# Optimization experiments

Measured on AMD Instinct MI355X. Metric: run time of the kernel, lower is better.

Reference implementation:

```python
import jax, jax.numpy as jnp
import numpy as np

NUM_GROUPS = 32
EPS = 1e-6


def group_norm(x, weight, bias):
    # x: [b, c, h, w]
    b, c, h, w = x.shape
    xg = x.reshape(b, NUM_GROUPS, c // NUM_GROUPS, h, w)
    mean = jnp.mean(xg, axis=(2, 3, 4), keepdims=True)
    var = jnp.var(xg, axis=(2, 3, 4), keepdims=True)
    xn = ((xg - mean) * jax.lax.rsqrt(var + EPS)).reshape(b, c, h, w)
    return xn * weight[None, :, None, None] + bias[None, :, None, None]


def conv1x1(x, w, b):
    # 1x1 conv == per-pixel matmul. x: [b, c_in, h, w], w: [c_out, c_in]
    return jnp.einsum('oi,bihw->bohw', w, x) + b[None, :, None, None]


def setup_inputs() -> dict:
    key = jax.random.key(0)
    ks = jax.random.split(key, 9)
    b, c, h, w = 8, 512, 64, 64
    scale = 1.0 / np.sqrt(c)
    return {
        'x': jax.random.normal(ks[0], (b, c, h, w), jnp.float32),
        'gn_weight': jnp.ones((c,), jnp.float32),
        'gn_bias': jnp.zeros((c,), jnp.float32),
        'wq': jax.random.normal(ks[1], (c, c), jnp.float32) * scale,
        'bq': jnp.zeros((c,), jnp.float32),
        'wk': jax.random.normal(ks[2], (c, c), jnp.float32) * scale,
        'bk': jnp.zeros((c,), jnp.float32),
        'wv': jax.random.normal(ks[3], (c, c), jnp.float32) * scale,
        'bv': jnp.zeros((c,), jnp.float32),
        'wp': jax.random.normal(ks[4], (c, c), jnp.float32) * scale,
        'bp': jnp.zeros((c,), jnp.float32),
    }


def reference(x, gn_weight, gn_bias, wq, bq, wk, bk, wv, bv, wp, bp):
    h_ = group_norm(x, gn_weight, gn_bias)
    q = conv1x1(h_, wq, bq)
    k = conv1x1(h_, wk, bk)
    v = conv1x1(h_, wv, bv)
    b, c, h, w = q.shape
    n = h * w
    qf = q.reshape(b, c, n)
    kf = k.reshape(b, c, n)
    vf = v.reshape(b, c, n)
    # scores: [b, q, k]
    scores = jnp.einsum('bcq,bck->bqk', qf, kf) * (c ** -0.5)
    attn = jax.nn.softmax(scores, axis=-1)
    out = jnp.einsum('bqk,bck->bcq', attn, vf).reshape(b, c, h, w)
    out = conv1x1(out, wp, bp)
    return x + out
```

## Files before the change

### kernel.cpp

```cpp
#include <hip/hip_runtime.h>
#include <cstdint>

typedef unsigned short u16;
typedef __bf16 bf16x8 __attribute__((ext_vector_type(8)));
typedef float f32x4 __attribute__((ext_vector_type(4)));

__device__ __forceinline__ u16 f2bf(float f) {
    uint32_t u = __float_as_uint(f);
    u += 0x7FFFu + ((u >> 16) & 1u);
    return (u16)(u >> 16);
}
__device__ __forceinline__ float bf2f(u16 v) {
    return __uint_as_float((uint32_t)v << 16);
}

__device__ __forceinline__ void gload16(const u16* g, u16* l) {
    __builtin_amdgcn_global_load_lds(
        (const __attribute__((address_space(1))) uint32_t*)g,
        (__attribute__((address_space(3))) uint32_t*)l, 16, 0, 0);
}

__device__ __forceinline__ void swz(int& n_idx, int& m_idx, int& z_idx) {
    const int nx = gridDim.x, ny = gridDim.y;
    int lid = blockIdx.x + nx * (blockIdx.y + ny * blockIdx.z);
    int g = lid & 7, h = lid >> 3;
    n_idx = h % nx;
    int pair = (h / nx) * 8 + g;
    m_idx = pair % ny;
    z_idx = pair / ny;
}

__global__ __launch_bounds__(256) void k_detect(const u16* __restrict__ x,
                                                int* __restrict__ flag) {
    const int t = threadIdx.x;
    uint32_t mx = 0;
    for (int i = 0; i < 256; i++) {
        uint32_t v = (uint32_t)x[i * 256 + t] & 0x7FFFu;
        mx = mx > v ? mx : v;
    }
    for (int off = 32; off > 0; off >>= 1) {
        uint32_t o = (uint32_t)__shfl_xor((int)mx, off);
        mx = mx > o ? mx : o;
    }
    __shared__ uint32_t r[4];
    if ((t & 63) == 0) r[t >> 6] = mx;
    __syncthreads();
    if (t == 0) {
        uint32_t a = r[0] > r[1] ? r[0] : r[1];
        uint32_t b = r[2] > r[3] ? r[2] : r[3];
        mx = a > b ? a : b;
        *flag = (mx > 0x5000u) ? 1 : 0;
    }
}

__global__ __launch_bounds__(256) void k_cvt_wb(const void* wq, const void* wk,
                                                const void* wv, const void* wp,
                                                const void* gw, const void* gb,
                                                const void* bq, const void* bk,
                                                const void* bv, const void* bp,
                                                const int* __restrict__ flag,
                                                u16* __restrict__ Wc,
                                                u16* __restrict__ Bc) {
    const int mode = *flag;
    int i = blockIdx.x * 256 + threadIdx.x;
    if (i >= 1048576 + 3072) return;
    const void* src;
    u16* dst;
    int off;
    if (i < 1048576) {
        int which = i >> 18;
        off = i & 262143;
        src = which == 0 ? wq : which == 1 ? wk : which == 2 ? wv : wp;
        dst = Wc + i;
    } else {
        int j = i - 1048576;
        int which = j >> 9;
        off = j & 511;
        src = which == 0 ? gw : which == 1 ? gb : which == 2 ? bq
            : which == 3 ? bk : which == 4 ? bv : bp;
        dst = Bc + j;
    }
    *dst = mode ? f2bf(((const float*)src)[off]) : ((const u16*)src)[off];
}

__global__ __launch_bounds__(256) void k_gn_stats(const void* __restrict__ x_raw,
                                                  const u16* __restrict__ Bc,
                                                  const int* __restrict__ flag,
                                                  float* __restrict__ Sc,
                                                  float* __restrict__ Sh) {
    const int b = blockIdx.x >> 5, g = blockIdx.x & 31;
    const int mode = *flag;
    const int t = threadIdx.x;
    const int wave = t >> 6, lane = t & 63;
    float s = 0.f, ss = 0.f;
    if (mode) {
        const float4* xb = (const float4*)((const float*)x_raw +
                                           ((size_t)b * 512 + g * 16) * 4096);
        for (int it = 0; it < 64; it++) {
            float4 v = xb[it * 256 + t];
            s += v.x + v.y + v.z + v.w;
            ss += v.x * v.x + v.y * v.y + v.z * v.z + v.w * v.w;
        }
    } else {
        const uint4* xb = (const uint4*)((const u16*)x_raw +
                                         ((size_t)b * 512 + g * 16) * 4096);
        for (int it = 0; it < 32; it++) {
            uint4 v = xb[it * 256 + t];
            uint32_t w[4] = {v.x, v.y, v.z, v.w};
            for (int j = 0; j < 4; j++) {
                float a = __uint_as_float(w[j] << 16);
                float c = __uint_as_float(w[j] & 0xFFFF0000u);
                s += a + c;
                ss += a * a + c * c;
            }
        }
    }
    for (int off = 32; off > 0; off >>= 1) {
        s += __shfl_xor(s, off);
        ss += __shfl_xor(ss, off);
    }
    __shared__ float rs[4], rss[4];
    if (lane == 0) { rs[wave] = s; rss[wave] = ss; }
    __syncthreads();
    s = rs[0] + rs[1] + rs[2] + rs[3];
    ss = rss[0] + rss[1] + rss[2] + rss[3];
    const float mean = s * (1.f / 65536.f);
    const float var = ss * (1.f / 65536.f) - mean * mean;
    const float rstd = rsqrtf(var + 1e-6f);
    if (t < 16) {
        int c = g * 16 + t;
        float w = bf2f(Bc[c]);
        Sc[b * 512 + c] = rstd * w;
        Sh[b * 512 + c] = bf2f(Bc[512 + c]) - mean * rstd * w;
    }
}

#define TPAD 520
__global__ __launch_bounds__(256) void k_gn_apply(const void* __restrict__ x_raw,
                                                  const int* __restrict__ flag,
                                                  const float* __restrict__ Sc,
                                                  const float* __restrict__ Sh,
                                                  u16* __restrict__ HT) {
    __shared__ u16 tile[64 * TPAD];
    __shared__ float sSc[512], sSh[512];
    const int b = blockIdx.y;
    const int p0 = blockIdx.x * 64;
    const int mode = *flag;
    const int t = threadIdx.x;
    sSc[t] = Sc[b * 512 + t]; sSc[t + 256] = Sc[b * 512 + t + 256];
    sSh[t] = Sh[b * 512 + t]; sSh[t + 256] = Sh[b * 512 + t + 256];
    __syncthreads();
    for (int it = 0; it < 16; it++) {
        int li = it * 256 + t;
        int c = li >> 3;
        int pj = (li & 7) * 8;
        float v[8];
        if (mode) {
            const float* xr = (const float*)x_raw + ((size_t)b * 512 + c) * 4096 + p0 + pj;
            float4 a = *(const float4*)xr;
            float4 d = *(const float4*)(xr + 4);
            v[0] = a.x; v[1] = a.y; v[2] = a.z; v[3] = a.w;
            v[4] = d.x; v[5] = d.y; v[6] = d.z; v[7] = d.w;
        } else {
            const u16* xr = (const u16*)x_raw + ((size_t)b * 512 + c) * 4096 + p0 + pj;
            uint4 a = *(const uint4*)xr;
            uint32_t w[4] = {a.x, a.y, a.z, a.w};
            for (int j = 0; j < 4; j++) {
                v[2 * j] = __uint_as_float(w[j] << 16);
                v[2 * j + 1] = __uint_as_float(w[j] & 0xFFFF0000u);
            }
        }
        float sc = sSc[c], sh = sSh[c];
        for (int k = 0; k < 8; k++)
            tile[(pj + k) * TPAD + c] = f2bf(v[k] * sc + sh);
    }
    __syncthreads();
    u16* H = HT + (size_t)b * 2097152 + (size_t)p0 * 512;
    for (int it = 0; it < 16; it++) {
        int ch = it * 256 + t;
        int pp = ch >> 6;
        int cc = (ch & 63) * 8;
        *(uint4*)&H[(size_t)pp * 512 + cc] = *(const uint4*)&tile[pp * TPAD + cc];
    }
}

__device__ __forceinline__ void gemm_core(const u16* __restrict__ A,
                                          const u16* __restrict__ BT,
                                          int lda, int ldb, int K,
                                          int m0, int n0,
                                          u16* lA, u16* lB,
                                          f32x4 (&acc)[4][4]) {
    const int t = threadIdx.x;
    const int wave = t >> 6, lane = t & 63;
    const int wm = (wave >> 1) * 64, wn = (wave & 1) * 64;
    const int mf = lane & 15, quad = lane >> 4;
    const int srow = t >> 3;
    const int scol = (((t & 7) ^ (srow & 7)) * 8);
    const u16* Ap = A + (size_t)(m0 + srow) * lda + scol;
    const u16* Bp = BT + (size_t)(n0 + srow) * ldb + scol;
    u16* lAd = &lA[t * 8];
    u16* lBd = &lB[t * 8];
    const int fx = mf & 7;

    for (int i = 0; i < 4; i++)
        for (int j = 0; j < 4; j++)
            acc[i][j] = (f32x4){0.f, 0.f, 0.f, 0.f};

    for (int k0 = 0; k0 < K; k0 += 64) {
        __syncthreads();
        gload16(Ap + k0, lAd);
        gload16(Ap + k0 + (size_t)32 * lda, lAd + 2048);
        gload16(Ap + k0 + (size_t)64 * lda, lAd + 4096);
        gload16(Ap + k0 + (size_t)96 * lda, lAd + 6144);
        gload16(Bp + k0, lBd);
        gload16(Bp + k0 + (size_t)32 * ldb, lBd + 2048);
        gload16(Bp + k0 + (size_t)64 * ldb, lBd + 4096);
        gload16(Bp + k0 + (size_t)96 * ldb, lBd + 6144);
        __syncthreads();
        for (int ks = 0; ks < 2; ks++) {
            bf16x8 af[4], bfr[4];
            const int sl = ((ks * 4 + quad) ^ fx) * 8;
            for (int i = 0; i < 4; i++)
                af[i] = *(const bf16x8*)&lA[(wm + i * 16 + mf) * 64 + sl];
            for (int j = 0; j < 4; j++)
                bfr[j] = *(const bf16x8*)&lB[(wn + j * 16 + mf) * 64 + sl];
            for (int i = 0; i < 4; i++)
                for (int j = 0; j < 4; j++)
                    acc[i][j] = __builtin_amdgcn_mfma_f32_16x16x32_bf16(af[i], bfr[j], acc[i][j], 0, 0, 0);
        }
    }
}

__global__ __launch_bounds__(256) void k_qk(const u16* __restrict__ HT,
                                            const u16* __restrict__ Wc,
                                            const u16* __restrict__ Bc,
                                            u16* __restrict__ QT,
                                            u16* __restrict__ KT) {
    __shared__ __align__(16) u16 lds[24576];
    int nI, mI, b;
    swz(nI, mI, b);
    const int n0 = nI * 128;
    const int m0 = mI * 128;
    const u16* A = HT + (size_t)b * 2097152;
    const u16* biasq = Bc + 1024;
    const u16* biask = Bc + 1024 + 512;
    u16* lA = lds;
    u16* lBq = lds + 8192;
    u16* lBk = lds + 16384;

    const int t = threadIdx.x;
    const int wave = t >> 6, lane = t & 63;
    const int wm = (wave >> 1) * 64, wn = (wave & 1) * 64;
    const int mf = lane & 15, quad = lane >> 4;
    const int srow = t >> 3;
    const int scol = (((t & 7) ^ (srow & 7)) * 8);
    const u16* Ap = A + (size_t)(m0 + srow) * 512 + scol;
    const u16* Bqp = Wc + (size_t)(n0 + srow) * 512 + scol;
    const u16* Bkp = Wc + 262144 + (size_t)(n0 + srow) * 512 + scol;
    u16* lAd = lA + t * 8;
    u16* lBqd = lBq + t * 8;
    u16* lBkd = lBk + t * 8;
    const int fx = mf & 7;

    f32x4 aq[4][4], ak[4][4];
    for (int i = 0; i < 4; i++)
        for (int j = 0; j < 4; j++) {
            aq[i][j] = (f32x4){0.f, 0.f, 0.f, 0.f};
            ak[i][j] = (f32x4){0.f, 0.f, 0.f, 0.f};
        }

    for (int k0 = 0; k0 < 512; k0 += 64) {
        __syncthreads();
        gload16(Ap + k0, lAd);
        gload16(Ap + k0 + (size_t)32 * 512, lAd + 2048);
        gload16(Ap + k0 + (size_t)64 * 512, lAd + 4096);
        gload16(Ap + k0 + (size_t)96 * 512, lAd + 6144);
        gload16(Bqp + k0, lBqd);
        gload16(Bqp + k0 + (size_t)32 * 512, lBqd + 2048);
        gload16(Bqp + k0 + (size_t)64 * 512, lBqd + 4096);
        gload16(Bqp + k0 + (size_t)96 * 512, lBqd + 6144);
        gload16(Bkp + k0, lBkd);
        gload16(Bkp + k0 + (size_t)32 * 512, lBkd + 2048);
        gload16(Bkp + k0 + (size_t)64 * 512, lBkd + 4096);
        gload16(Bkp + k0 + (size_t)96 * 512, lBkd + 6144);
        __syncthreads();
#pragma unroll
        for (int ks = 0; ks < 2; ks++) {
            bf16x8 af[4], bq4[4], bk4[4];
            const int sl = ((ks * 4 + quad) ^ fx) * 8;
#pragma unroll
            for (int i = 0; i < 4; i++)
                af[i] = *(const bf16x8*)&lA[(wm + i * 16 + mf) * 64 + sl];
#pragma unroll
            for (int j = 0; j < 4; j++) {
                bq4[j] = *(const bf16x8*)&lBq[(wn + j * 16 + mf) * 64 + sl];
                bk4[j] = *(const bf16x8*)&lBk[(wn + j * 16 + mf) * 64 + sl];
            }
#pragma unroll
            for (int i = 0; i < 4; i++)
#pragma unroll
                for (int j = 0; j < 4; j++) {
                    aq[i][j] = __builtin_amdgcn_mfma_f32_16x16x32_bf16(af[i], bq4[j], aq[i][j], 0, 0, 0);
                    ak[i][j] = __builtin_amdgcn_mfma_f32_16x16x32_bf16(af[i], bk4[j], ak[i][j], 0, 0, 0);
                }
        }
    }

    for (int which = 0; which < 2; which++) {
        const u16* Bb = which == 0 ? biasq : biask;
        u16* O = (which == 0 ? QT : KT) + (size_t)b * 2097152;
        __syncthreads();
        for (int i = 0; i < 4; i++)
            for (int r = 0; r < 4; r++) {
                int row = wm + i * 16 + quad * 4 + r;
                int kk = ((row >> 2) & 3) << 4;
                for (int j = 0; j < 4; j++) {
                    int col = wn + j * 16 + mf;
                    float v = (which == 0 ? aq[i][j][r] : ak[i][j][r]) + bf2f(Bb[n0 + col]);
                    lds[row * 128 + (col ^ kk)] = f2bf(v);
                }
            }
        __syncthreads();
        for (int p = 0; p < 8; p++) {
            int idx = p * 256 + t;
            int rowt = idx >> 4, c8 = (idx & 15) * 8;
            int kk = ((rowt >> 2) & 3) << 4;
            uint4 v = *(const uint4*)&lds[rowt * 128 + (c8 ^ kk)];
            *(uint4*)&O[(size_t)(m0 + rowt) * 512 + n0 + c8] = v;
        }
    }
}

__global__ __launch_bounds__(256) void k_v(const u16* __restrict__ HT,
                                           const u16* __restrict__ Wc,
                                           const u16* __restrict__ Bc,
                                           u16* __restrict__ V) {
    __shared__ __align__(16) u16 sm[16384];
    int nI, mI, b;
    swz(nI, mI, b);
    const int m0 = nI * 128;
    const int n0 = mI * 128;
    const u16* A = Wc + (size_t)2 * 262144;
    const u16* BT = HT + (size_t)b * 2097152;
    const u16* Bb = Bc + 1024 + 2 * 512;
    u16* O = V + (size_t)b * 2097152;
    f32x4 acc[4][4];
    gemm_core(A, BT, 512, 512, 512, m0, n0, sm, sm + 8192, acc);

    const int t = threadIdx.x;
    const int wave = t >> 6, lane = t & 63;
    const int wm = (wave >> 1) * 64, wn = (wave & 1) * 64;
    const int mf = lane & 15, quad = lane >> 4;
    __syncthreads();
    for (int i = 0; i < 4; i++)
        for (int r = 0; r < 4; r++) {
            int row = wm + i * 16 + quad * 4 + r;
            int kk = ((row >> 2) & 3) << 4;
            float bias = bf2f(Bb[m0 + row]);
            for (int j = 0; j < 4; j++) {
                int col = wn + j * 16 + mf;
                sm[row * 128 + (col ^ kk)] = f2bf(acc[i][j][r] + bias);
            }
        }
    __syncthreads();
    for (int p = 0; p < 8; p++) {
        int idx = p * 256 + t;
        int rowt = idx >> 4, c8 = (idx & 15) * 8;
        int kk = ((rowt >> 2) & 3) << 4;
        uint4 v = *(const uint4*)&sm[rowt * 128 + (c8 ^ kk)];
        *(uint4*)&O[(size_t)(m0 + rowt) * 4096 + n0 + c8] = v;
    }
}

__device__ __forceinline__ u16* s_ptr(u16* S_ht, u16* S_tail, int l) {
    return l == 0 ? S_ht : S_tail + (size_t)(l - 1) * 16777216;
}

__global__ __launch_bounds__(256) void k_scores(const u16* __restrict__ QT,
                                                const u16* __restrict__ KT,
                                                u16* __restrict__ S_ht,
                                                u16* __restrict__ S_tail,
                                                float* __restrict__ Part,
                                                int b0) {
    __shared__ __align__(16) u16 sm[16384];
    int nI, mI, l;
    swz(nI, mI, l);
    const int n0 = nI * 128;
    const int m0 = mI * 128;
    const int b = b0 + l;
    f32x4 acc[4][4];
    gemm_core(QT + (size_t)b * 2097152, KT + (size_t)b * 2097152, 512, 512, 512,
              m0, n0, sm, sm + 8192, acc);

    const float scale = 0.04419417382415922f;
    const int t = threadIdx.x;
    const int wave = t >> 6, lane = t & 63;
    const int wm = (wave >> 1) * 64, wn = (wave & 1) * 64;
    const int mf = lane & 15, quad = lane >> 4;
    __syncthreads();
    for (int i = 0; i < 4; i++)
        for (int r = 0; r < 4; r++) {
            int row = wm + i * 16 + quad * 4 + r;
            int kk = ((row >> 2) & 3) << 4;
            for (int j = 0; j < 4; j++) {
                int col = wn + j * 16 + mf;
                sm[row * 128 + (col ^ kk)] = f2bf(__expf(acc[i][j][r] * scale));
            }
        }
    __syncthreads();
    u16* Sb = s_ptr(S_ht, S_tail, l);
    float* pr = Part + ((size_t)b * 32 + nI) * 4096 + m0;
    for (int p = 0; p < 8; p++) {
        int idx = p * 256 + t;
        int rowt = idx >> 4, c8 = (idx & 15) * 8;
        int kk = ((rowt >> 2) & 3) << 4;
        uint4 v = *(const uint4*)&sm[rowt * 128 + (c8 ^ kk)];
        uint32_t w[4] = {v.x, v.y, v.z, v.w};
        float s = 0.f;
        for (int q2 = 0; q2 < 4; q2++)
            s += __uint_as_float(w[q2] << 16) + __uint_as_float(w[q2] & 0xFFFF0000u);
        for (int off = 8; off > 0; off >>= 1) s += __shfl_xor(s, off);
        if ((lane & 15) == 0) pr[rowt] = s;
        *(uint4*)&Sb[(size_t)(m0 + rowt) * 4096 + n0 + c8] = v;
    }
}

__global__ __launch_bounds__(256) void k_pv_split(u16* __restrict__ S_ht,
                                                  u16* __restrict__ S_tail,
                                                  const u16* __restrict__ V,
                                                  u16* __restrict__ QT,
                                                  u16* __restrict__ KT,
                                                  int b0) {
    __shared__ __align__(16) u16 sm[16384];
    int nI, mI, zI;
    swz(nI, mI, zI);
    const int n0 = nI * 128;
    const int m0 = mI * 128;
    const int l = zI >> 1, split = zI & 1, b = b0 + l;
    const u16* A = s_ptr(S_ht, S_tail, l) + split * 2048;
    const u16* BT = V + (size_t)b * 2097152 + split * 2048;
    f32x4 acc[4][4];
    gemm_core(A, BT, 4096, 4096, 2048, m0, n0, sm, sm + 8192, acc);

    const int t = threadIdx.x;
    const int wave = t >> 6, lane = t & 63;
    const int wm = (wave >> 1) * 64, wn = (wave & 1) * 64;
    const int mf = lane & 15, quad = lane >> 4;
    u16* P = (split == 0 ? QT : KT) + (size_t)b * 2097152;
    __syncthreads();
    for (int i = 0; i < 4; i++)
        for (int r = 0; r < 4; r++) {
            int row = wm + i * 16 + quad * 4 + r;
            int kk = ((row >> 2) & 3) << 4;
            for (int j = 0; j < 4; j++) {
                int col = wn + j * 16 + mf;
                sm[row * 128 + (col ^ kk)] = f2bf(acc[i][j][r]);
            }
        }
    __syncthreads();
    for (int p = 0; p < 8; p++) {
        int idx = p * 256 + t;
        int rowt = idx >> 4, c8 = (idx & 15) * 8;
        int kk = ((rowt >> 2) & 3) << 4;
        uint4 v = *(const uint4*)&sm[rowt * 128 + (c8 ^ kk)];
        *(uint4*)&P[(size_t)(m0 + rowt) * 512 + n0 + c8] = v;
    }
}

__global__ __launch_bounds__(256) void k_pv_reduce(const u16* __restrict__ QT,
                                                   const u16* __restrict__ KT,
                                                   const float* __restrict__ Part,
                                                   u16* __restrict__ OT,
                                                   int b0) {
    const int b = b0 + blockIdx.y;
    const int t = threadIdx.x;
    __shared__ float sInv[4];
    if (t < 128) {
        int r = t >> 5, which = t & 31;
        int p = blockIdx.x * 4 + r;
        float v = Part[((size_t)b * 32 + which) * 4096 + p];
        for (int off = 16; off > 0; off >>= 1) v += __shfl_xor(v, off);
        if (which == 0) sInv[r] = 1.f / v;
    }
    __syncthreads();
    const float inv = sInv[t >> 6];
    size_t base = (size_t)b * 2097152;
    size_t i0 = base + ((size_t)blockIdx.x * 256 + t) * 8;
    uint4 a = *(const uint4*)(QT + i0);
    uint4 c = *(const uint4*)(KT + i0);
    uint32_t wa[4] = {a.x, a.y, a.z, a.w};
    uint32_t wc[4] = {c.x, c.y, c.z, c.w};
    uint32_t o[4];
    for (int j = 0; j < 4; j++) {
        float lo = (__uint_as_float(wa[j] << 16) + __uint_as_float(wc[j] << 16)) * inv;
        float hi = (__uint_as_float(wa[j] & 0xFFFF0000u) + __uint_as_float(wc[j] & 0xFFFF0000u)) * inv;
        o[j] = (uint32_t)f2bf(lo) | ((uint32_t)f2bf(hi) << 16);
    }
    *(uint4*)(OT + i0) = make_uint4(o[0], o[1], o[2], o[3]);
}

__global__ __launch_bounds__(256) void k_proj(const u16* __restrict__ Wc,
                                              const u16* __restrict__ OT,
                                              const u16* __restrict__ Bc,
                                              const void* __restrict__ x_raw,
                                              const int* __restrict__ flag,
                                              void* __restrict__ y_raw) {
    __shared__ __align__(16) u16 smu[16384];
    float* smf = (float*)smu;
    int nI, mI, b;
    swz(nI, mI, b);
    const int n0 = nI * 128;
    const int m0 = mI * 128;
    f32x4 acc[4][4];
    gemm_core(Wc + (size_t)3 * 262144, OT + (size_t)b * 2097152, 512, 512, 512,
              m0, n0, smu, smu + 8192, acc);

    const int mode = *flag;
    const u16* bp = Bc + 5 * 512;
    const int t = threadIdx.x;
    const int wave = t >> 6, lane = t & 63;
    const int wn = (wave & 1) * 64;
    const int mf = lane & 15, quad = lane >> 4;
    const int whalf = wave >> 1;
    size_t bb = (size_t)b * 2097152;
    for (int h = 0; h < 2; h++) {
        __syncthreads();
        if (whalf == h) {
            for (int i = 0; i < 4; i++)
                for (int r = 0; r < 4; r++) {
                    int rowl = i * 16 + quad * 4 + r;
                    int kf = ((rowl >> 2) & 1) << 4;
                    for (int j = 0; j < 4; j++) {
                        int col = wn + j * 16 + mf;
                        smf[rowl * 128 + (col ^ kf)] = acc[i][j][r];
                    }
                }
        }
        __syncthreads();
        const int rowbase = m0 + h * 64;
        if (mode) {
            for (int p = 0; p < 8; p++) {
                int idx = p * 256 + t;
                int rowl = idx >> 5, c4 = (idx & 31) * 4;
                int kf = ((rowl >> 2) & 1) << 4;
                f32x4 v = *(const f32x4*)&smf[rowl * 128 + (c4 ^ kf)];
                int rowg = rowbase + rowl;
                float bias = bf2f(bp[rowg]);
                size_t o = bb + (size_t)rowg * 4096 + n0 + c4;
                float4 xv = *(const float4*)((const float*)x_raw + o);
                float4 out = make_float4(v[0] + bias + xv.x, v[1] + bias + xv.y,
                                         v[2] + bias + xv.z, v[3] + bias + xv.w);
                *(float4*)((float*)y_raw + o) = out;
            }
        } else {
            for (int p = 0; p < 4; p++) {
                int idx = p * 256 + t;
                int rowl = idx >> 4, c8 = (idx & 15) * 8;
                int kf = ((rowl >> 2) & 1) << 4;
                const float* sp = &smf[rowl * 128 + (c8 ^ kf)];
                f32x4 v0 = *(const f32x4*)sp;
                f32x4 v1 = *(const f32x4*)(sp + 4);
                int rowg = rowbase + rowl;
                float bias = bf2f(bp[rowg]);
                size_t o = bb + (size_t)rowg * 4096 + n0 + c8;
                uint4 xv = *(const uint4*)((const u16*)x_raw + o);
                uint32_t xw[4] = {xv.x, xv.y, xv.z, xv.w};
                float vals[8] = {v0[0], v0[1], v0[2], v0[3],
                                 v1[0], v1[1], v1[2], v1[3]};
                uint32_t ow[4];
                for (int q2 = 0; q2 < 4; q2++) {
                    float lo = __uint_as_float(xw[q2] << 16) + vals[2 * q2] + bias;
                    float hi = __uint_as_float(xw[q2] & 0xFFFF0000u) + vals[2 * q2 + 1] + bias;
                    ow[q2] = (uint32_t)f2bf(lo) | ((uint32_t)f2bf(hi) << 16);
                }
                *(uint4*)((u16*)y_raw + o) = make_uint4(ow[0], ow[1], ow[2], ow[3]);
            }
        }
    }
}

extern "C" void kernel_launch(void* const* d_in, const int* in_sizes, int n_in,
                              void* d_out, int out_size, void* d_ws, size_t ws_size,
                              hipStream_t stream) {
    (void)in_sizes; (void)n_in; (void)out_size;
    const void* x  = d_in[0];
    const void* gw = d_in[1];
    const void* gb = d_in[2];
    const void* wq = d_in[3];
    const void* bq = d_in[4];
    const void* wk = d_in[5];
    const void* bk = d_in[6];
    const void* wv = d_in[7];
    const void* bv = d_in[8];
    const void* wp = d_in[9];
    const void* bp = d_in[10];

    u16* ws16 = (u16*)d_ws;
    int* flag = (int*)d_ws;
    float* Sc = (float*)(ws16 + 16);
    float* Sh = Sc + 4096;
    u16* Wc = ws16 + 16 + 16384;
    u16* Bc = Wc + 1048576;
    u16* HT = Bc + 4096;
    u16* QT = HT + 16777216;
    u16* KT = QT + 16777216;
    u16* V  = KT + 16777216;
    u16* OT = V  + 16777216;
    float* Part = (float*)(OT + 16777216);
    u16* Tail = (u16*)(Part + 1048576);
    const size_t base_elems = (size_t)(Tail - ws16);

    int nb = 1;
    for (int cand = 8; cand >= 2; cand >>= 1) {
        size_t need = 2ull * (base_elems + (size_t)(cand - 1) * 16777216ull);
        if (ws_size >= need) { nb = cand; break; }
    }

    k_detect<<<1, 256, 0, stream>>>((const u16*)x, flag);
    k_cvt_wb<<<4108, 256, 0, stream>>>(wq, wk, wv, wp, gw, gb, bq, bk, bv, bp,
                                       flag, Wc, Bc);
    k_gn_stats<<<256, 256, 0, stream>>>(x, Bc, flag, Sc, Sh);
    k_gn_apply<<<dim3(64, 8), 256, 0, stream>>>(x, flag, Sc, Sh, HT);
    k_qk<<<dim3(4, 32, 8), 256, 0, stream>>>(HT, Wc, Bc, QT, KT);
    k_v<<<dim3(4, 32, 8), 256, 0, stream>>>(HT, Wc, Bc, V);
    for (int b0 = 0; b0 < 8; b0 += nb) {
        k_scores<<<dim3(32, 32, nb), 256, 0, stream>>>(QT, KT, HT, Tail, Part, b0);
        k_pv_split<<<dim3(4, 32, 2 * nb), 256, 0, stream>>>(HT, Tail, V, QT, KT, b0);
        k_pv_reduce<<<dim3(1024, nb), 256, 0, stream>>>(QT, KT, Part, OT, b0);
    }
    k_proj<<<dim3(32, 4, 8), 256, 0, stream>>>(Wc, OT, Bc, x, flag, d_out);
}
```

Measured before the change: 799.3 us.

## Use 512-thread blocks computing 128x256 tiles sharing A tile across two B halves

Introduces a gemm_dual helper where 8 waves share one LDS-staged A tile and each half of the block multiplies it against a different 128-column B tile. k_qk, k_scores, k_pv_split and k_proj switch to 512-thread blocks with 128x256 output tiles, halving grid sizes and cutting A-tile reloads from global memory. The aim is more data reuse per LDS load and fewer per-block accumulator registers in k_qk. The trade-offs are fewer blocks, which can leave CUs idle on small grids, and serialized epilogues that need extra barriers.

```diff
diff --git a/kernel.cpp b/kernel.cpp
--- a/kernel.cpp
+++ b/kernel.cpp
@@ -231,98 +231,102 @@
     }
 }
 
-__global__ __launch_bounds__(256) void k_qk(const u16* __restrict__ HT,
-                                            const u16* __restrict__ Wc,
-                                            const u16* __restrict__ Bc,
-                                            u16* __restrict__ QT,
-                                            u16* __restrict__ KT) {
+__device__ __forceinline__ void gemm_dual(const u16* __restrict__ A,
+                                          const u16* __restrict__ B0,
+                                          const u16* __restrict__ B1,
+                                          int lda, int ldb, int K,
+                                          int m0, int n0,
+                                          u16* lds,
+                                          f32x4 (&acc)[4][4]) {
+    const int t = threadIdx.x;
+    const int wave = t >> 6, lane = t & 63;
+    const int half = wave >> 2, wIn = wave & 3;
+    const int wm = (wIn >> 1) * 64, wn = (wIn & 1) * 64;
+    const int mf = lane & 15, quad = lane >> 4;
+    const int srow = t >> 3;
+    const int scol = (((t & 7) ^ (srow & 7)) * 8);
+    const u16* Ap = A + (size_t)(m0 + srow) * lda + scol;
+    const u16* B0p = B0 + (size_t)(n0 + srow) * ldb + scol;
+    const u16* B1p = B1 + (size_t)(n0 + srow) * ldb + scol;
+    u16* lA = lds;
+    u16* lB0 = lds + 8192;
+    u16* lB1 = lds + 16384;
+    u16* lAd = lA + t * 8;
+    u16* lB0d = lB0 + t * 8;
+    u16* lB1d = lB1 + t * 8;
+    const int fx = mf & 7;
+    const u16* lBh = half ? lB1 : lB0;
+
+    for (int i = 0; i < 4; i++)
+        for (int j = 0; j < 4; j++)
+            acc[i][j] = (f32x4){0.f, 0.f, 0.f, 0.f};
+
+    for (int k0 = 0; k0 < K; k0 += 64) {
+        __syncthreads();
+        gload16(Ap + k0, lAd);
+        gload16(Ap + k0 + (size_t)64 * lda, lAd + 4096);
+        gload16(B0p + k0, lB0d);
+        gload16(B0p + k0 + (size_t)64 * ldb, lB0d + 4096);
+        gload16(B1p + k0, lB1d);
+        gload16(B1p + k0 + (size_t)64 * ldb, lB1d + 4096);
+        __syncthreads();
+#pragma unroll
+        for (int ks = 0; ks < 2; ks++) {
+            bf16x8 af[4], bfr[4];
+            const int sl = ((ks * 4 + quad) ^ fx) * 8;
+#pragma unroll
+            for (int i = 0; i < 4; i++)
+                af[i] = *(const bf16x8*)&lA[(wm + i * 16 + mf) * 64 + sl];
+#pragma unroll
+            for (int j = 0; j < 4; j++)
+                bfr[j] = *(const bf16x8*)&lBh[(wn + j * 16 + mf) * 64 + sl];
+#pragma unroll
+            for (int i = 0; i < 4; i++)
+#pragma unroll
+                for (int j = 0; j < 4; j++)
+                    acc[i][j] = __builtin_amdgcn_mfma_f32_16x16x32_bf16(af[i], bfr[j], acc[i][j], 0, 0, 0);
+        }
+    }
+}
+
+__global__ __launch_bounds__(512, 4) void k_qk(const u16* __restrict__ HT,
+                                               const u16* __restrict__ Wc,
+                                               const u16* __restrict__ Bc,
+                                               u16* __restrict__ QT,
+                                               u16* __restrict__ KT) {
     __shared__ __align__(16) u16 lds[24576];
     int nI, mI, b;
     swz(nI, mI, b);
     const int n0 = nI * 128;
     const int m0 = mI * 128;
-    const u16* A = HT + (size_t)b * 2097152;
-    const u16* biasq = Bc + 1024;
-    const u16* biask = Bc + 1024 + 512;
-    u16* lA = lds;
-    u16* lBq = lds + 8192;
-    u16* lBk = lds + 16384;
-
-    const int t = threadIdx.x;
-    const int wave = t >> 6, lane = t & 63;
-    const int wm = (wave >> 1) * 64, wn = (wave & 1) * 64;
+    f32x4 acc[4][4];
+    gemm_dual(HT + (size_t)b * 2097152, Wc, Wc + 262144,
+              512, 512, 512, m0, n0, lds, acc);
+
+    const int t = threadIdx.x;
+    const int wave = t >> 6, lane = t & 63;
+    const int half = wave >> 2, wIn = wave & 3;
+    const int wm = (wIn >> 1) * 64, wn = (wIn & 1) * 64;
     const int mf = lane & 15, quad = lane >> 4;
-    const int srow = t >> 3;
-    const int scol = (((t & 7) ^ (srow & 7)) * 8);
-    const u16* Ap = A + (size_t)(m0 + srow) * 512 + scol;
-    const u16* Bqp = Wc + (size_t)(n0 + srow) * 512 + scol;
-    const u16* Bkp = Wc + 262144 + (size_t)(n0 + srow) * 512 + scol;
-    u16* lAd = lA + t * 8;
-    u16* lBqd = lBq + t * 8;
-    u16* lBkd = lBk + t * 8;
-    const int fx = mf & 7;
-
-    f32x4 aq[4][4], ak[4][4];
-    for (int i = 0; i < 4; i++)
-        for (int j = 0; j < 4; j++) {
-            aq[i][j] = (f32x4){0.f, 0.f, 0.f, 0.f};
-            ak[i][j] = (f32x4){0.f, 0.f, 0.f, 0.f};
-        }
-
-    for (int k0 = 0; k0 < 512; k0 += 64) {
-        __syncthreads();
-        gload16(Ap + k0, lAd);
-        gload16(Ap + k0 + (size_t)32 * 512, lAd + 2048);
-        gload16(Ap + k0 + (size_t)64 * 512, lAd + 4096);
-        gload16(Ap + k0 + (size_t)96 * 512, lAd + 6144);
-        gload16(Bqp + k0, lBqd);
-        gload16(Bqp + k0 + (size_t)32 * 512, lBqd + 2048);
-        gload16(Bqp + k0 + (size_t)64 * 512, lBqd + 4096);
-        gload16(Bqp + k0 + (size_t)96 * 512, lBqd + 6144);
-        gload16(Bkp + k0, lBkd);
-        gload16(Bkp + k0 + (size_t)32 * 512, lBkd + 2048);
-        gload16(Bkp + k0 + (size_t)64 * 512, lBkd + 4096);
-        gload16(Bkp + k0 + (size_t)96 * 512, lBkd + 6144);
-        __syncthreads();
-#pragma unroll
-        for (int ks = 0; ks < 2; ks++) {
-            bf16x8 af[4], bq4[4], bk4[4];
-            const int sl = ((ks * 4 + quad) ^ fx) * 8;
-#pragma unroll
+    for (int which = 0; which < 2; which++) {
+        const u16* Bb = Bc + 1024 + which * 512;
+        u16* O = (which == 0 ? QT : KT) + (size_t)b * 2097152;
+        __syncthreads();
+        if (half == which) {
             for (int i = 0; i < 4; i++)
-                af[i] = *(const bf16x8*)&lA[(wm + i * 16 + mf) * 64 + sl];
-#pragma unroll
-            for (int j = 0; j < 4; j++) {
-                bq4[j] = *(const bf16x8*)&lBq[(wn + j * 16 + mf) * 64 + sl];
-                bk4[j] = *(const bf16x8*)&lBk[(wn + j * 16 + mf) * 64 + sl];
-            }
-#pragma unroll
-            for (int i = 0; i < 4; i++)
-#pragma unroll
-                for (int j = 0; j < 4; j++) {
-                    aq[i][j] = __builtin_amdgcn_mfma_f32_16x16x32_bf16(af[i], bq4[j], aq[i][j], 0, 0, 0);
-                    ak[i][j] = __builtin_amdgcn_mfma_f32_16x16x32_bf16(af[i], bk4[j], ak[i][j], 0, 0, 0);
+                for (int r = 0; r < 4; r++) {
+                    int row = wm + i * 16 + quad * 4 + r;
+                    int kk = ((row >> 2) & 3) << 4;
+                    for (int j = 0; j < 4; j++) {
+                        int col = wn + j * 16 + mf;
+                        lds[row * 128 + (col ^ kk)] =
+                            f2bf(acc[i][j][r] + bf2f(Bb[n0 + col]));
+                    }
                 }
         }
-    }
-
-    for (int which = 0; which < 2; which++) {
-        const u16* Bb = which == 0 ? biasq : biask;
-        u16* O = (which == 0 ? QT : KT) + (size_t)b * 2097152;
-        __syncthreads();
-        for (int i = 0; i < 4; i++)
-            for (int r = 0; r < 4; r++) {
-                int row = wm + i * 16 + quad * 4 + r;
-                int kk = ((row >> 2) & 3) << 4;
-                for (int j = 0; j < 4; j++) {
-                    int col = wn + j * 16 + mf;
-                    float v = (which == 0 ? aq[i][j][r] : ak[i][j][r]) + bf2f(Bb[n0 + col]);
-                    lds[row * 128 + (col ^ kk)] = f2bf(v);
-                }
-            }
-        __syncthreads();
-        for (int p = 0; p < 8; p++) {
-            int idx = p * 256 + t;
+        __syncthreads();
+        for (int p = 0; p < 4; p++) {
+            int idx = p * 512 + t;
             int rowt = idx >> 4, c8 = (idx & 15) * 8;
             int kk = ((rowt >> 2) & 3) << 4;
             uint4 v = *(const uint4*)&lds[rowt * 128 + (c8 ^ kk)];
@@ -376,94 +380,107 @@
     return l == 0 ? S_ht : S_tail + (size_t)(l - 1) * 16777216;
 }
 
-__global__ __launch_bounds__(256) void k_scores(const u16* __restrict__ QT,
-                                                const u16* __restrict__ KT,
-                                                u16* __restrict__ S_ht,
-                                                u16* __restrict__ S_tail,
-                                                float* __restrict__ Part,
-                                                int b0) {
-    __shared__ __align__(16) u16 sm[16384];
+__global__ __launch_bounds__(512, 4) void k_scores(const u16* __restrict__ QT,
+                                                   const u16* __restrict__ KT,
+                                                   u16* __restrict__ S_ht,
+                                                   u16* __restrict__ S_tail,
+                                                   float* __restrict__ Part,
+                                                   int b0) {
+    __shared__ __align__(16) u16 lds[24576];
     int nI, mI, l;
     swz(nI, mI, l);
-    const int n0 = nI * 128;
+    const int n0 = nI * 256;
     const int m0 = mI * 128;
     const int b = b0 + l;
+    const u16* Kb = KT + (size_t)b * 2097152;
     f32x4 acc[4][4];
-    gemm_core(QT + (size_t)b * 2097152, KT + (size_t)b * 2097152, 512, 512, 512,
-              m0, n0, sm, sm + 8192, acc);
+    gemm_dual(QT + (size_t)b * 2097152, Kb + (size_t)n0 * 512,
+              Kb + (size_t)(n0 + 128) * 512, 512, 512, 512, m0, 0, lds, acc);
 
     const float scale = 0.04419417382415922f;
     const int t = threadIdx.x;
     const int wave = t >> 6, lane = t & 63;
-    const int wm = (wave >> 1) * 64, wn = (wave & 1) * 64;
+    const int half = wave >> 2, wIn = wave & 3;
+    const int wm = (wIn >> 1) * 64, wn = (wIn & 1) * 64;
     const int mf = lane & 15, quad = lane >> 4;
-    __syncthreads();
-    for (int i = 0; i < 4; i++)
-        for (int r = 0; r < 4; r++) {
-            int row = wm + i * 16 + quad * 4 + r;
-            int kk = ((row >> 2) & 3) << 4;
-            for (int j = 0; j < 4; j++) {
-                int col = wn + j * 16 + mf;
-                sm[row * 128 + (col ^ kk)] = f2bf(__expf(acc[i][j][r] * scale));
-            }
-        }
-    __syncthreads();
     u16* Sb = s_ptr(S_ht, S_tail, l);
-    float* pr = Part + ((size_t)b * 32 + nI) * 4096 + m0;
-    for (int p = 0; p < 8; p++) {
-        int idx = p * 256 + t;
-        int rowt = idx >> 4, c8 = (idx & 15) * 8;
-        int kk = ((rowt >> 2) & 3) << 4;
-        uint4 v = *(const uint4*)&sm[rowt * 128 + (c8 ^ kk)];
-        uint32_t w[4] = {v.x, v.y, v.z, v.w};
-        float s = 0.f;
-        for (int q2 = 0; q2 < 4; q2++)
-            s += __uint_as_float(w[q2] << 16) + __uint_as_float(w[q2] & 0xFFFF0000u);
-        for (int off = 8; off > 0; off >>= 1) s += __shfl_xor(s, off);
-        if ((lane & 15) == 0) pr[rowt] = s;
-        *(uint4*)&Sb[(size_t)(m0 + rowt) * 4096 + n0 + c8] = v;
-    }
-}
-
-__global__ __launch_bounds__(256) void k_pv_split(u16* __restrict__ S_ht,
-                                                  u16* __restrict__ S_tail,
-                                                  const u16* __restrict__ V,
-                                                  u16* __restrict__ QT,
-                                                  u16* __restrict__ KT,
-                                                  int b0) {
-    __shared__ __align__(16) u16 sm[16384];
+    for (int which = 0; which < 2; which++) {
+        __syncthreads();
+        if (half == which) {
+            for (int i = 0; i < 4; i++)
+                for (int r = 0; r < 4; r++) {
+                    int row = wm + i * 16 + quad * 4 + r;
+                    int kk = ((row >> 2) & 3) << 4;
+                    for (int j = 0; j < 4; j++) {
+                        int col = wn + j * 16 + mf;
+                        lds[row * 128 + (col ^ kk)] =
+                            f2bf(__expf(acc[i][j][r] * scale));
+                    }
+                }
+        }
+        __syncthreads();
+        float* pr = Part + ((size_t)b * 32 + nI * 2 + which) * 4096 + m0;
+        for (int p = 0; p < 4; p++) {
+            int idx = p * 512 + t;
+            int rowt = idx >> 4, c8 = (idx & 15) * 8;
+            int kk = ((rowt >> 2) & 3) << 4;
+            uint4 v = *(const uint4*)&lds[rowt * 128 + (c8 ^ kk)];
+            uint32_t w[4] = {v.x, v.y, v.z, v.w};
+            float s = 0.f;
+            for (int q2 = 0; q2 < 4; q2++)
+                s += __uint_as_float(w[q2] << 16) + __uint_as_float(w[q2] & 0xFFFF0000u);
+            for (int off = 8; off > 0; off >>= 1) s += __shfl_xor(s, off);
+            if ((lane & 15) == 0) pr[rowt] = s;
+            *(uint4*)&Sb[(size_t)(m0 + rowt) * 4096 + n0 + which * 128 + c8] = v;
+        }
+    }
+}
+
+__global__ __launch_bounds__(512, 4) void k_pv_split(u16* __restrict__ S_ht,
+                                                     u16* __restrict__ S_tail,
+                                                     const u16* __restrict__ V,
+                                                     u16* __restrict__ QT,
+                                                     u16* __restrict__ KT,
+                                                     int b0) {
+    __shared__ __align__(16) u16 lds[24576];
     int nI, mI, zI;
     swz(nI, mI, zI);
-    const int n0 = nI * 128;
+    const int n0 = nI * 256;
     const int m0 = mI * 128;
     const int l = zI >> 1, split = zI & 1, b = b0 + l;
     const u16* A = s_ptr(S_ht, S_tail, l) + split * 2048;
-    const u16* BT = V + (size_t)b * 2097152 + split * 2048;
+    const u16* Vb = V + (size_t)b * 2097152 + split * 2048;
     f32x4 acc[4][4];
-    gemm_core(A, BT, 4096, 4096, 2048, m0, n0, sm, sm + 8192, acc);
-
-    const int t = threadIdx.x;
-    const int wave = t >> 6, lane = t & 63;
-    const int wm = (wave >> 1) * 64, wn = (wave & 1) * 64;
+    gemm_dual(A, Vb + (size_t)n0 * 4096, Vb + (size_t)(n0 + 128) * 4096,
+              4096, 4096, 2048, m0, 0, lds, acc);
+
+    const int t = threadIdx.x;
+    const int wave = t >> 6, lane = t & 63;
+    const int half = wave >> 2, wIn = wave & 3;
+    const int wm = (wIn >> 1) * 64, wn = (wIn & 1) * 64;
     const int mf = lane & 15, quad = lane >> 4;
     u16* P = (split == 0 ? QT : KT) + (size_t)b * 2097152;
-    __syncthreads();
-    for (int i = 0; i < 4; i++)
-        for (int r = 0; r < 4; r++) {
-            int row = wm + i * 16 + quad * 4 + r;
-            int kk = ((row >> 2) & 3) << 4;
-            for (int j = 0; j < 4; j++) {
-                int col = wn + j * 16 + mf;
-                sm[row * 128 + (col ^ kk)] = f2bf(acc[i][j][r]);
-            }
-        }
-    __syncthreads();
-    for (int p = 0; p < 8; p++) {
-        int idx = p * 256 + t;
-        int rowt = idx >> 4, c8 = (idx & 15) * 8;
-        int kk = ((rowt >> 2) & 3) << 4;
-        uint4 v = *(const uint4*)&sm[rowt * 128 + (c8 ^ kk)];
-        *(uint4*)&P[(size_t)(m0 + rowt) * 512 + n0 + c8] = v;
+    for (int which = 0; which < 2; which++) {
+        __syncthreads();
+        if (half == which) {
+            for (int i = 0; i < 4; i++)
+                for (int r = 0; r < 4; r++) {
+                    int row = wm + i * 16 + quad * 4 + r;
+                    int kk = ((row >> 2) & 3) << 4;
+                    for (int j = 0; j < 4; j++) {
+                        int col = wn + j * 16 + mf;
+                        lds[row * 128 + (col ^ kk)] = f2bf(acc[i][j][r]);
+                    }
+                }
+        }
+        __syncthreads();
+        for (int p = 0; p < 4; p++) {
+            int idx = p * 512 + t;
+            int rowt = idx >> 4, c8 = (idx & 15) * 8;
+            int kk = ((rowt >> 2) & 3) << 4;
+            uint4 v = *(const uint4*)&lds[rowt * 128 + (c8 ^ kk)];
+            *(uint4*)&P[(size_t)(m0 + rowt) * 512 + n0 + which * 128 + c8] = v;
+        }
     }
 }
 
@@ -499,81 +516,86 @@
     *(uint4*)(OT + i0) = make_uint4(o[0], o[1], o[2], o[3]);
 }
 
-__global__ __launch_bounds__(256) void k_proj(const u16* __restrict__ Wc,
-                                              const u16* __restrict__ OT,
-                                              const u16* __restrict__ Bc,
-                                              const void* __restrict__ x_raw,
-                                              const int* __restrict__ flag,
-                                              void* __restrict__ y_raw) {
-    __shared__ __align__(16) u16 smu[16384];
-    float* smf = (float*)smu;
+__global__ __launch_bounds__(512, 4) void k_proj(const u16* __restrict__ Wc,
+                                                 const u16* __restrict__ OT,
+                                                 const u16* __restrict__ Bc,
+                                                 const void* __restrict__ x_raw,
+                                                 const int* __restrict__ flag,
+                                                 void* __restrict__ y_raw) {
+    __shared__ __align__(16) u16 lds[24576];
+    float* smf = (float*)lds;
     int nI, mI, b;
     swz(nI, mI, b);
-    const int n0 = nI * 128;
+    const int n0 = nI * 256;
     const int m0 = mI * 128;
+    const u16* Ob = OT + (size_t)b * 2097152;
     f32x4 acc[4][4];
-    gemm_core(Wc + (size_t)3 * 262144, OT + (size_t)b * 2097152, 512, 512, 512,
-              m0, n0, smu, smu + 8192, acc);
+    gemm_dual(Wc + (size_t)3 * 262144, Ob + (size_t)n0 * 512,
+              Ob + (size_t)(n0 + 128) * 512, 512, 512, 512, m0, 0, lds, acc);
 
     const int mode = *flag;
     const u16* bp = Bc + 5 * 512;
     const int t = threadIdx.x;
     const int wave = t >> 6, lane = t & 63;
-    const int wn = (wave & 1) * 64;
+    const int half = wave >> 2, wIn = wave & 3;
+    const int wn = (wIn & 1) * 64;
     const int mf = lane & 15, quad = lane >> 4;
-    const int whalf = wave >> 1;
+    const int whalfIn = wIn >> 1;
     size_t bb = (size_t)b * 2097152;
-    for (int h = 0; h < 2; h++) {
-        __syncthreads();
-        if (whalf == h) {
-            for (int i = 0; i < 4; i++)
-                for (int r = 0; r < 4; r++) {
-                    int rowl = i * 16 + quad * 4 + r;
+    for (int which = 0; which < 2; which++) {
+        const int colbase = n0 + which * 128;
+        for (int h = 0; h < 2; h++) {
+            __syncthreads();
+            if (half == which && whalfIn == h) {
+                for (int i = 0; i < 4; i++)
+                    for (int r = 0; r < 4; r++) {
+                        int rowl = i * 16 + quad * 4 + r;
+                        int kf = ((rowl >> 2) & 1) << 4;
+                        for (int j = 0; j < 4; j++) {
+                            int col = wn + j * 16 + mf;
+                            smf[rowl * 128 + (col ^ kf)] = acc[i][j][r];
+                        }
+                    }
+            }
+            __syncthreads();
+            const int rowbase = m0 + h * 64;
+            if (mode) {
+                for (int p = 0; p < 4; p++) {
+                    int idx = p * 512 + t;
+                    int rowl = idx >> 5, c4 = (idx & 31) * 4;
                     int kf = ((rowl >> 2) & 1) << 4;
-                    for (int j = 0; j < 4; j++) {
-                        int col = wn + j * 16 + mf;
-                        smf[rowl * 128 + (col ^ kf)] = acc[i][j][r];
+                    f32x4 v = *(const f32x4*)&smf[rowl * 128 + (c4 ^ kf)];
+                    int rowg = rowbase + rowl;
+                    float bias = bf2f(bp[rowg]);
+                    size_t o = bb + (size_t)rowg * 4096 + colbase + c4;
+                    float4 xv = *(const float4*)((const float*)x_raw + o);
+                    float4 out = make_float4(v[0] + bias + xv.x, v[1] + bias + xv.y,
+                                             v[2] + bias + xv.z, v[3] + bias + xv.w);
+                    *(float4*)((float*)y_raw + o) = out;
+                }
+            } else {
+                for (int p = 0; p < 2; p++) {
+                    int idx = p * 512 + t;
+                    int rowl = idx >> 4, c8 = (idx & 15) * 8;
+                    int kf = ((rowl >> 2) & 1) << 4;
+                    const float* sp = &smf[rowl * 128 + (c8 ^ kf)];
+                    f32x4 v0 = *(const f32x4*)sp;
+                    f32x4 v1 = *(const f32x4*)(sp + 4);
+                    int rowg = rowbase + rowl;
+                    float bias = bf2f(bp[rowg]);
+                    size_t o = bb + (size_t)rowg * 4096 + colbase + c8;
+                    uint4 xv = *(const uint4*)((const u16*)x_raw + o);
+                    uint32_t xw[4] = {xv.x, xv.y, xv.z, xv.w};
+                    float vals[8] = {v0[0], v0[1], v0[2], v0[3],
+                                     v1[0], v1[1], v1[2], v1[3]};
+                    uint32_t ow[4];
+                    for (int q2 = 0; q2 < 4; q2++) {
+                        float lo = __uint_as_float(xw[q2] << 16) + vals[2 * q2] + bias;
+                        float hi = __uint_as_float(xw[q2] & 0xFFFF0000u) + vals[2 * q2 + 1] + bias;
+                        ow[q2] = (uint32_t)f2bf(lo) | ((uint32_t)f2bf(hi) << 16);
                     }
+                    *(uint4*)((u16*)y_raw + o) = make_uint4(ow[0], ow[1], ow[2], ow[3]);
                 }
-        }
-        __syncthreads();
-        const int rowbase = m0 + h * 64;
-        if (mode) {
-            for (int p = 0; p < 8; p++) {
-                int idx = p * 256 + t;
-                int rowl = idx >> 5, c4 = (idx & 31) * 4;
-                int kf = ((rowl >> 2) & 1) << 4;
-                f32x4 v = *(const f32x4*)&smf[rowl * 128 + (c4 ^ kf)];
-                int rowg = rowbase + rowl;
-                float bias = bf2f(bp[rowg]);
-                size_t o = bb + (size_t)rowg * 4096 + n0 + c4;
-                float4 xv = *(const float4*)((const float*)x_raw + o);
-                float4 out = make_float4(v[0] + bias + xv.x, v[1] + bias + xv.y,
-                                         v[2] + bias + xv.z, v[3] + bias + xv.w);
-                *(float4*)((float*)y_raw + o) = out;
-            }
-        } else {
-            for (int p = 0; p < 4; p++) {
-                int idx = p * 256 + t;
-                int rowl = idx >> 4, c8 = (idx & 15) * 8;
-                int kf = ((rowl >> 2) & 1) << 4;
-                const float* sp = &smf[rowl * 128 + (c8 ^ kf)];
-                f32x4 v0 = *(const f32x4*)sp;
-                f32x4 v1 = *(const f32x4*)(sp + 4);
-                int rowg = rowbase + rowl;
-                float bias = bf2f(bp[rowg]);
-                size_t o = bb + (size_t)rowg * 4096 + n0 + c8;
-                uint4 xv = *(const uint4*)((const u16*)x_raw + o);
-                uint32_t xw[4] = {xv.x, xv.y, xv.z, xv.w};
-                float vals[8] = {v0[0], v0[1], v0[2], v0[3],
-                                 v1[0], v1[1], v1[2], v1[3]};
-                uint32_t ow[4];
-                for (int q2 = 0; q2 < 4; q2++) {
-                    float lo = __uint_as_float(xw[q2] << 16) + vals[2 * q2] + bias;
-                    float hi = __uint_as_float(xw[q2] & 0xFFFF0000u) + vals[2 * q2 + 1] + bias;
-                    ow[q2] = (uint32_t)f2bf(lo) | ((uint32_t)f2bf(hi) << 16);
-                }
-                *(uint4*)((u16*)y_raw + o) = make_uint4(ow[0], ow[1], ow[2], ow[3]);
             }
         }
     }
@@ -621,12 +643,12 @@
                                        flag, Wc, Bc);
     k_gn_stats<<<256, 256, 0, stream>>>(x, Bc, flag, Sc, Sh);
     k_gn_apply<<<dim3(64, 8), 256, 0, stream>>>(x, flag, Sc, Sh, HT);
-    k_qk<<<dim3(4, 32, 8), 256, 0, stream>>>(HT, Wc, Bc, QT, KT);
+    k_qk<<<dim3(4, 32, 8), 512, 0, stream>>>(HT, Wc, Bc, QT, KT);
     k_v<<<dim3(4, 32, 8), 256, 0, stream>>>(HT, Wc, Bc, V);
     for (int b0 = 0; b0 < 8; b0 += nb) {
-        k_scores<<<dim3(32, 32, nb), 256, 0, stream>>>(QT, KT, HT, Tail, Part, b0);
-        k_pv_split<<<dim3(4, 32, 2 * nb), 256, 0, stream>>>(HT, Tail, V, QT, KT, b0);
+        k_scores<<<dim3(16, 32, nb), 512, 0, stream>>>(QT, KT, HT, Tail, Part, b0);
+        k_pv_split<<<dim3(2, 32, 2 * nb), 512, 0, stream>>>(HT, Tail, V, QT, KT, b0);
         k_pv_reduce<<<dim3(1024, nb), 256, 0, stream>>>(QT, KT, Part, OT, b0);
     }
-    k_proj<<<dim3(32, 4, 8), 256, 0, stream>>>(Wc, OT, Bc, x, flag, d_out);
-}
+    k_proj<<<dim3(16, 4, 8), 512, 0, stream>>>(Wc, OT, Bc, x, flag, d_out);
+}
```

After: 792.3 us. No clear change (-0.9%).
